# Performance work log

Hardware: AMD Instinct MI355X
Metric: run time of the kernel (lower is better)

## Reference

```python
import jax, jax.numpy as jnp
import numpy as np

L = 4       # num_fourier_layers
W = 256     # width
NF = 256    # num_freq (no_low_freq)
B = 2       # batch size
N = 16384   # num_nodes per graph
E = 524288  # total edges (avg degree 16)
D_IN = 3    # darcy input features


def lin(x, w, b):
    # torch nn.Linear convention: w is (out, in)
    return x @ w.T + b


def layernorm(x, s, b):
    m = x.mean(-1, keepdims=True)
    v = x.var(-1, keepdims=True)
    return (x - m) / jnp.sqrt(v + 1e-5) * s + b


def setup_inputs() -> dict:
    key = jax.random.key(0)
    ks = jax.random.split(key, 16)
    s = lambda i, shape, sc=0.05: sc * jax.random.normal(ks[i], shape, jnp.float32)
    inp = {
        "x": jax.random.normal(ks[0], (B * N, D_IN), jnp.float32),
        "U": jax.random.normal(ks[1], (B, N, NF), jnp.float32) / np.float32(np.sqrt(N)),
        "edge_index": jax.random.randint(ks[2], (2, E), 0, B * N),
        "edge_weight": jax.random.uniform(ks[3], (E,), jnp.float32),
        "lif_embed": jax.random.normal(ks[4], (B * N, 16), jnp.float32),
        "p_w": s(5, (W, D_IN)), "p_b": jnp.zeros((W,), jnp.float32),
        # scale = 1/(in*out) * rand, per GraphFourierLayer
        "four_w": (1.0 / (W * W)) * jax.random.uniform(ks[6], (L, W, W, NF), jnp.float32),
        "w_w": s(7, (L, W, W)), "w_b": jnp.zeros((L, W), jnp.float32),
        "ln_s": jnp.ones((L, W), jnp.float32), "ln_b": jnp.zeros((L, W), jnp.float32),
        "lin_w": s(8, (L, W, W)), "lin_b": jnp.zeros((L, W), jnp.float32),
        "ew_w": s(9, (L, 16, 1)), "ew_b": jnp.zeros((L, 16), jnp.float32),
        "g1_w": s(10, (L, 3, 48)), "g1_b": jnp.zeros((L, 3), jnp.float32),
        "g2_w": s(11, (L, 1, 3)), "g2_b": jnp.zeros((L, 1), jnp.float32),
        "proj_w": s(12, (W, 2 * W)), "proj_b": jnp.zeros((W,), jnp.float32),
        "q1_w": s(13, (128, W)), "q1_b": jnp.zeros((128,), jnp.float32),
        "q2_w": s(14, (1, 128)), "q2_b": jnp.zeros((1,), jnp.float32),
    }
    return inp


def reference(x, U, edge_index, edge_weight, lif_embed,
              p_w, p_b, four_w, w_w, w_b, ln_s, ln_b,
              lin_w, lin_b, ew_w, ew_b, g1_w, g1_b, g2_w, g2_b,
              proj_w, proj_b, q1_w, q1_b, q2_w, q2_b):
    src = edge_index[0]  # edge_index_j (source)
    dst = edge_index[1]  # edge_index_i (target, aggr='add')
    h = lin(x, p_w, p_b)  # [B*N, W]

    for l in range(L):
        # --- GraphFourierLayer: batched spectral transform ---
        h3 = h.reshape(B, N, W)
        x_ft = jnp.einsum('bnf,bnw->bfw', U, h3)          # U^T x  -> [B, NF, W]
        out_ft = jnp.einsum('bfi,iof->bfo', x_ft, four_w[l])
        x1 = jnp.einsum('bnf,bfw->bnw', U, out_ft).reshape(B * N, W)
        xf = jax.nn.gelu(x1 + lin(h, w_w[l], w_b[l]), approximate=False)
        xf = layernorm(xf, ln_s[l], ln_b[l])

        # --- FrigateConv: gather -> edge MLP gate -> scatter-add -> L2 normalize ---
        xs = lin(h, lin_w[l], lin_b[l])
        ew = lin(edge_weight[:, None], ew_w[l], ew_b[l])  # [E, 16]
        gin = jnp.concatenate([ew, lif_embed[dst], lif_embed[src]], axis=1)  # [E, 48]
        g = jax.nn.sigmoid(lin(jax.nn.relu(lin(gin, g1_w[l], g1_b[l])), g2_w[l], g2_b[l]))
        msg = xs[src] * g                                  # [E, W]
        agg = jax.ops.segment_sum(msg, dst, num_segments=B * N)
        nrm = jnp.maximum(jnp.linalg.norm(agg, axis=-1, keepdims=True), 1e-12)
        xs = agg / nrm

        h = lin(jnp.concatenate([xf, xs], axis=1), proj_w, proj_b)

    out = lin(jax.nn.relu(lin(h, q1_w, q1_b)), q2_w, q2_b)  # q: MLP(W,1,128)
    return out
```

## Files before the change

kernel.cpp:

```cpp
#include <hip/hip_runtime.h>
#include <hip/hip_bf16.h>

#define B_ 2
#define N_ 16384
#define BN 32768
#define W_ 256
#define NF_ 256
#define E_ 524288
#define L_ 4
#define KS_ 32

typedef __attribute__((ext_vector_type(8))) short bf16x8;
typedef __attribute__((ext_vector_type(4))) float f32x4;

__device__ __forceinline__ unsigned short f2b(float x) {
    __hip_bfloat16 h = __float2bfloat16(x);
    return *reinterpret_cast<unsigned short*>(&h);
}
__device__ __forceinline__ float b2f(unsigned short u) {
    union { unsigned int i; float f; } c; c.i = ((unsigned int)u) << 16; return c.f;
}
__device__ __forceinline__ float geluf(float x) {
    return 0.5f * x * (1.0f + erff(x * 0.70710678118654752440f));
}

template<bool DUAL, int OUTM, bool BIAS, bool QHEAD = false, bool TROUT = false>
__global__ __launch_bounds__(256) void k_mfma_nt(
    const unsigned short* __restrict__ A1, int lda1, long A1o, long A1i,
    const unsigned short* __restrict__ B1, int ldb1, long B1o, long B1i, int K1,
    const unsigned short* __restrict__ A2, int lda2, long A2o,
    const unsigned short* __restrict__ B2, int ldb2, long B2o, int K2,
    void* __restrict__ Cv, int ldc, long Co, long Ci,
    unsigned short* __restrict__ CT,
    const float* __restrict__ bias,
    const float* __restrict__ qw, const float* __restrict__ q2b,
    float* __restrict__ qout, int zdiv)
{
    __shared__ unsigned short lds[16384];
    const int t = threadIdx.x;
    const int wid = t >> 6, lane = t & 63;
    const int wr = wid >> 1, wc = wid & 1;
    const int m0 = blockIdx.y * 128, n0 = blockIdx.x * 128;
    const int z = blockIdx.z;
    const int zo = z / zdiv, zi = z - zo * zdiv;
    A1 += zo * A1o + zi * A1i;
    B1 += zo * B1o + zi * B1i;
    if (DUAL) { A2 += zo * A2o; B2 += zo * B2o; }

    const int srow  = t >> 3;
    const int sgran = (t & 7) ^ (srow & 7);
    const int rlo   = lane & 15;
    const int hi    = lane >> 4;

    f32x4 acc[4][4] = {};

    const int nph = DUAL ? 2 : 1;
    for (int ph = 0; ph < nph; ++ph) {
        const unsigned short* A  = (DUAL && ph) ? A2 : A1;
        const unsigned short* Bp = (DUAL && ph) ? B2 : B1;
        const int lda = (DUAL && ph) ? lda2 : lda1;
        const int ldb = (DUAL && ph) ? ldb2 : ldb1;
        const int K   = (DUAL && ph) ? K2 : K1;
        for (int k0 = 0; k0 < K; k0 += 64) {
            __syncthreads();
            #pragma unroll
            for (int j = 0; j < 4; ++j) {
                const unsigned short* ga = A + (long)(m0 + j*32 + srow) * lda + k0 + sgran*8;
                __builtin_amdgcn_global_load_lds(
                    (const __attribute__((address_space(1))) void*)ga,
                    (__attribute__((address_space(3))) void*)&lds[(j*4 + wid) * 512],
                    16, 0, 0);
            }
            #pragma unroll
            for (int j = 0; j < 4; ++j) {
                const unsigned short* gb = Bp + (long)(n0 + j*32 + srow) * ldb + k0 + sgran*8;
                __builtin_amdgcn_global_load_lds(
                    (const __attribute__((address_space(1))) void*)gb,
                    (__attribute__((address_space(3))) void*)&lds[8192 + (j*4 + wid) * 512],
                    16, 0, 0);
            }
            __syncthreads();
            #pragma unroll
            for (int kk = 0; kk < 2; ++kk) {
                const int g8 = (((kk*4 + hi) ^ (lane & 7)) << 3);
                bf16x8 a[4], b[4];
                #pragma unroll
                for (int fm = 0; fm < 4; ++fm)
                    a[fm] = *(const bf16x8*)&lds[(wr*64 + fm*16 + rlo)*64 + g8];
                #pragma unroll
                for (int fn = 0; fn < 4; ++fn)
                    b[fn] = *(const bf16x8*)&lds[8192 + (wc*64 + fn*16 + rlo)*64 + g8];
                #pragma unroll
                for (int fm = 0; fm < 4; ++fm)
                    #pragma unroll
                    for (int fn = 0; fn < 4; ++fn)
                        acc[fm][fn] = __builtin_amdgcn_mfma_f32_16x16x32_bf16(
                            a[fm], b[fn], acc[fm][fn], 0, 0, 0);
            }
        }
    }

    const int mb = m0 + wr*64, nb = n0 + wc*64;
    if (QHEAD) {
        __syncthreads();
        float* rs = (float*)lds;
        if (t < 128) rs[t] = 0.f;
        __syncthreads();
        #pragma unroll
        for (int fm = 0; fm < 4; ++fm)
            #pragma unroll
            for (int r = 0; r < 4; ++r) {
                const int m_l = wr*64 + fm*16 + hi*4 + r;
                float part = 0.f;
                #pragma unroll
                for (int fn = 0; fn < 4; ++fn) {
                    const int n = nb + fn*16 + rlo;
                    part += fmaxf(acc[fm][fn][r] + bias[n], 0.f) * qw[n];
                }
                #pragma unroll
                for (int o = 8; o; o >>= 1) part += __shfl_xor(part, o);
                if (rlo == 0) atomicAdd(&rs[m_l], part);
            }
        __syncthreads();
        if (t < 128) qout[m0 + t] = rs[t] + q2b[0];
    } else if (OUTM == 1) {
        unsigned short* C = (unsigned short*)Cv + zo * Co + zi * Ci;
        #pragma unroll
        for (int fn = 0; fn < 4; ++fn) {
            const int n = nb + fn*16 + rlo;
            const float bv = BIAS ? bias[n] : 0.f;
            #pragma unroll
            for (int fm = 0; fm < 4; ++fm)
                #pragma unroll
                for (int r = 0; r < 4; ++r) {
                    const int m = mb + fm*16 + hi*4 + r;
                    C[(long)m*ldc + n] = f2b(acc[fm][fn][r] + bv);
                }
        }
        if (TROUT) {
            __syncthreads();
            unsigned short* wlds = &lds[wid * 4096];
            #pragma unroll
            for (int fm = 0; fm < 4; ++fm)
                #pragma unroll
                for (int r = 0; r < 4; ++r) {
                    const int m_l = fm*16 + hi*4 + r;
                    const int sw = (m_l & 7) << 3;
                    #pragma unroll
                    for (int fn = 0; fn < 4; ++fn) {
                        const int n_l = fn*16 + rlo;
                        const float bv = BIAS ? bias[nb + n_l] : 0.f;
                        wlds[m_l*64 + (n_l ^ sw)] = f2b(acc[fm][fn][r] + bv);
                    }
                }
            const int bb = mb >> 14, loc = mb & 16383;
            const int mq = lane & 15, nq = lane >> 4;
            #pragma unroll
            for (int p = 0; p < 16; ++p) {
                const int n_l = p*4 + nq;
                unsigned short v[4];
                #pragma unroll
                for (int j = 0; j < 4; ++j) {
                    const int m_l = mq*4 + j;
                    v[j] = wlds[m_l*64 + (n_l ^ ((m_l & 7) << 3))];
                }
                *(ushort4*)&CT[((long)bb*ldc + nb + n_l)*N_ + loc + mq*4] = *(ushort4*)v;
            }
        }
    } else {
        float* C = (float*)Cv + zo * Co + zi * Ci;
        #pragma unroll
        for (int fn = 0; fn < 4; ++fn) {
            const int n = nb + fn*16 + rlo;
            const float bv = BIAS ? bias[n] : 0.f;
            #pragma unroll
            for (int fm = 0; fm < 4; ++fm)
                #pragma unroll
                for (int r = 0; r < 4; ++r) {
                    const int m = mb + fm*16 + hi*4 + r;
                    C[(long)m*ldc + n] = acc[fm][fn][r] + bv;
                }
        }
    }
}

__global__ __launch_bounds__(256) void k_cvt_all(
    const float* __restrict__ w, const float* __restrict__ lin,
    const float* __restrict__ proj, const float* __restrict__ q1,
    unsigned short* __restrict__ wd, unsigned short* __restrict__ lind,
    unsigned short* __restrict__ projd, unsigned short* __restrict__ q1d)
{
    const int b = blockIdx.x;
    const float* s; unsigned short* d; long base;
    if (b < 256)      { s = w;    d = wd;    base = (long)b * 1024; }
    else if (b < 512) { s = lin;  d = lind;  base = (long)(b-256) * 1024; }
    else if (b < 640) { s = proj; d = projd; base = (long)(b-512) * 1024; }
    else              { s = q1;   d = q1d;   base = (long)(b-640) * 1024; }
    long i = base + (long)threadIdx.x * 4;
    float4 v = *(const float4*)&s[i];
    ushort4 u = {f2b(v.x), f2b(v.y), f2b(v.z), f2b(v.w)};
    *(ushort4*)&d[i] = u;
}

__global__ __launch_bounds__(256) void k_cvtT(
    const float* __restrict__ src, unsigned short* __restrict__ dT, unsigned short* __restrict__ dL)
{
    const int b = blockIdx.z;
    src += (long)b * N_ * NF_; dT += (long)b * N_ * NF_; dL += (long)b * N_ * NF_;
    const int r0 = blockIdx.y * 64, c0 = blockIdx.x * 64;
    __shared__ unsigned short tile[64][72];
    const int t = threadIdx.x, lr = t >> 4, lc4 = (t & 15) * 4;
    #pragma unroll
    for (int p = 0; p < 4; ++p) {
        int r = p*16 + lr;
        float4 v = *(const float4*)&src[(long)(r0+r)*NF_ + c0 + lc4];
        ushort4 u = {f2b(v.x), f2b(v.y), f2b(v.z), f2b(v.w)};
        *(ushort4*)&dL[(long)(r0+r)*NF_ + c0 + lc4] = u;
        tile[r][lc4+0]=u.x; tile[r][lc4+1]=u.y; tile[r][lc4+2]=u.z; tile[r][lc4+3]=u.w;
    }
    __syncthreads();
    #pragma unroll
    for (int p = 0; p < 4; ++p) {
        int c = p*16 + lr;
        ushort4 u = {tile[lc4+0][c], tile[lc4+1][c], tile[lc4+2][c], tile[lc4+3][c]};
        *(ushort4*)&dT[(long)(c0+c)*N_ + r0 + lc4] = u;
    }
}

__global__ __launch_bounds__(256) void k_T_b2b(
    const unsigned short* __restrict__ src, unsigned short* __restrict__ dst)
{
    const int b = blockIdx.z;
    src += (long)b * N_ * W_; dst += (long)b * N_ * W_;
    const int r0 = blockIdx.y * 64, c0 = blockIdx.x * 64;
    __shared__ unsigned short tile[64][72];
    const int t = threadIdx.x, lr = t >> 4, lc4 = (t & 15) * 4;
    #pragma unroll
    for (int p = 0; p < 4; ++p) {
        int r = p*16 + lr;
        ushort4 v = *(const ushort4*)&src[(long)(r0+r)*W_ + c0 + lc4];
        tile[r][lc4+0]=v.x; tile[r][lc4+1]=v.y; tile[r][lc4+2]=v.z; tile[r][lc4+3]=v.w;
    }
    __syncthreads();
    #pragma unroll
    for (int p = 0; p < 4; ++p) {
        int c = p*16 + lr;
        ushort4 u = {tile[lc4+0][c], tile[lc4+1][c], tile[lc4+2][c], tile[lc4+3][c]};
        *(ushort4*)&dst[(long)(c0+c)*N_ + r0 + lc4] = u;
    }
}

__global__ __launch_bounds__(256) void k_in_proj(
    const float* __restrict__ x, const float* __restrict__ pw,
    const float* __restrict__ pb, unsigned short* __restrict__ h)
{
    int idx = blockIdx.x * 256 + threadIdx.x;
    int node = idx >> 8, w = idx & 255;
    float x0 = x[node*3+0], x1 = x[node*3+1], x2 = x[node*3+2];
    h[idx] = f2b(fmaf(x0, pw[w*3+0], fmaf(x1, pw[w*3+1], fmaf(x2, pw[w*3+2], pb[w]))));
}

__global__ __launch_bounds__(256) void k_reduce_ks(
    const float* __restrict__ part, float* __restrict__ outp)
{
    int idx = blockIdx.x * 256 + threadIdx.x;
    int b = idx >> 16, rem = idx & 65535;
    const float* p = part + (long)b * KS_ * 65536 + rem;
    float s = 0.f;
    #pragma unroll
    for (int k = 0; k < KS_; ++k) s += p[(long)k * 65536];
    outp[idx] = s;
}

__global__ __launch_bounds__(256) void k_fourier_mul(
    const float* __restrict__ fw, const float* __restrict__ xftT,
    unsigned short* __restrict__ oftT)
{
    const int o = blockIdx.x, f = threadIdx.x;
    const float* fwp = fw + (long)o * NF_ + f;
    float a0 = 0.f, a1 = 0.f;
    #pragma unroll 8
    for (int i = 0; i < W_; ++i) {
        float w = fwp[(long)i * W_ * NF_];
        a0 = fmaf(xftT[i*NF_ + f], w, a0);
        a1 = fmaf(xftT[65536 + i*NF_ + f], w, a1);
    }
    oftT[o*NF_ + f] = f2b(a0);
    oftT[65536 + o*NF_ + f] = f2b(a1);
}

__global__ __launch_bounds__(256) void k_gelu_ln(
    const unsigned short* __restrict__ xf, unsigned short* __restrict__ out,
    const float* __restrict__ wb, const float* __restrict__ lns, const float* __restrict__ lnb)
{
    const int node = blockIdx.x * 4 + (threadIdx.x >> 6);
    const int lane = threadIdx.x & 63;
    ushort4 v4 = *(const ushort4*)(xf + (long)node*W_ + lane*4);
    float4 bb = *(const float4*)(wb + lane*4);
    float e0 = geluf(b2f(v4.x)+bb.x), e1 = geluf(b2f(v4.y)+bb.y);
    float e2 = geluf(b2f(v4.z)+bb.z), e3 = geluf(b2f(v4.w)+bb.w);
    float s  = e0+e1+e2+e3;
    float s2 = e0*e0+e1*e1+e2*e2+e3*e3;
    #pragma unroll
    for (int o = 32; o; o >>= 1) { s += __shfl_xor(s, o); s2 += __shfl_xor(s2, o); }
    float mean = s * (1.0f/W_);
    float var  = s2 * (1.0f/W_) - mean*mean;
    float inv = rsqrtf(var + 1e-5f);
    float4 sc = *(const float4*)(lns + lane*4);
    float4 bi = *(const float4*)(lnb + lane*4);
    ushort4 o4;
    o4.x = f2b((e0-mean)*inv*sc.x + bi.x);
    o4.y = f2b((e1-mean)*inv*sc.y + bi.y);
    o4.z = f2b((e2-mean)*inv*sc.z + bi.z);
    o4.w = f2b((e3-mean)*inv*sc.w + bi.w);
    *(ushort4*)(out + (long)node*W_ + lane*4) = o4;
}

__global__ __launch_bounds__(256) void k_hist(const int* __restrict__ ei, int* __restrict__ count) {
    int e = blockIdx.x * 256 + threadIdx.x;
    atomicAdd(&count[ei[E_ + e]], 1);
}
__global__ __launch_bounds__(256) void k_scan(const int* __restrict__ count, int* __restrict__ offsets) {
    __shared__ int sums[256];
    const int t = threadIdx.x;
    const int base = t * 128;
    int s = 0;
    for (int i = 0; i < 128; ++i) s += count[base + i];
    sums[t] = s;
    __syncthreads();
    for (int off = 1; off < 256; off <<= 1) {
        int v = (t >= off) ? sums[t - off] : 0;
        __syncthreads();
        sums[t] += v;
        __syncthreads();
    }
    int run = (t == 0) ? 0 : sums[t - 1];
    for (int i = 0; i < 128; ++i) { offsets[base + i] = run; run += count[base + i]; }
    if (t == 255) offsets[BN] = run;
}
__global__ __launch_bounds__(256) void k_place(
    const int* __restrict__ ei, const float* __restrict__ ewt,
    const int* __restrict__ offsets, int* __restrict__ cursor,
    int* __restrict__ srcp, float* __restrict__ ewt_p)
{
    int e = blockIdx.x * 256 + threadIdx.x;
    int dst = ei[E_ + e];
    int pos = offsets[dst] + atomicAdd(&cursor[dst], 1);
    srcp[pos] = ei[e];
    ewt_p[pos] = ewt[e];
}

__global__ __launch_bounds__(256) void k_gate_agg(
    const int* __restrict__ offsets, const int* __restrict__ srcp,
    const float* __restrict__ ewt_p, const float* __restrict__ lif,
    const float* __restrict__ eww, const float* __restrict__ ewb,
    const float* __restrict__ g1w, const float* __restrict__ g1b,
    const float* __restrict__ g2w, const float* __restrict__ g2b,
    const unsigned short* __restrict__ xs, unsigned short* __restrict__ out)
{
    const int node = blockIdx.x * 4 + (threadIdx.x >> 6);
    const int lane = threadIdx.x & 63;
    const int beg = offsets[node], end = offsets[node + 1];
    float lifd[16];
    #pragma unroll
    for (int j = 0; j < 16; ++j) lifd[j] = lif[node*16 + j];
    float a0=0.f, a1=0.f, a2=0.f, a3=0.f;
    for (int c0 = beg; c0 < end; c0 += 64) {
        const int p = c0 + lane;
        float gate = 0.f; int src = 0;
        if (p < end) {
            src = srcp[p];
            const float wv = ewt_p[p];
            float t0 = g1b[0], t1 = g1b[1], t2 = g1b[2];
            #pragma unroll
            for (int j = 0; j < 16; ++j) {
                const float e0 = fmaf(wv, eww[j], ewb[j]);
                const float l1 = lifd[j];
                const float l2 = lif[src*16 + j];
                t0 = fmaf(g1w[j], e0, t0);
                t0 = fmaf(g1w[16 + j], l1, t0);
                t0 = fmaf(g1w[32 + j], l2, t0);
                t1 = fmaf(g1w[48 + j], e0, t1);
                t1 = fmaf(g1w[64 + j], l1, t1);
                t1 = fmaf(g1w[80 + j], l2, t1);
                t2 = fmaf(g1w[96 + j], e0, t2);
                t2 = fmaf(g1w[112 + j], l1, t2);
                t2 = fmaf(g1w[128 + j], l2, t2);
            }
            float z = g2b[0];
            z = fmaf(g2w[0], fmaxf(t0, 0.f), z);
            z = fmaf(g2w[1], fmaxf(t1, 0.f), z);
            z = fmaf(g2w[2], fmaxf(t2, 0.f), z);
            gate = 1.f / (1.f + __expf(-z));
        }
        const int m = min(64, end - c0);
        for (int j = 0; j < m; ++j) {
            const float gv = __shfl(gate, j);
            const int   s  = __shfl(src, j);
            ushort4 v = *(const ushort4*)&xs[(long)s * W_ + lane * 4];
            a0 = fmaf(b2f(v.x), gv, a0);
            a1 = fmaf(b2f(v.y), gv, a1);
            a2 = fmaf(b2f(v.z), gv, a2);
            a3 = fmaf(b2f(v.w), gv, a3);
        }
    }
    float s = a0*a0 + a1*a1 + a2*a2 + a3*a3;
    #pragma unroll
    for (int o = 32; o; o >>= 1) s += __shfl_xor(s, o);
    float inv = 1.f / fmaxf(sqrtf(s), 1e-12f);
    ushort4 r = {f2b(a0*inv), f2b(a1*inv), f2b(a2*inv), f2b(a3*inv)};
    *(ushort4*)(out + (long)node * W_ + lane * 4) = r;
}

extern "C" void kernel_launch(void* const* d_in, const int* in_sizes, int n_in,
                              void* d_out, int out_size, void* d_ws, size_t ws_size,
                              hipStream_t stream)
{
    const float* x      = (const float*)d_in[0];
    const float* U      = (const float*)d_in[1];
    const int*   ei     = (const int*)  d_in[2];
    const float* ewt    = (const float*)d_in[3];
    const float* lif    = (const float*)d_in[4];
    const float* p_w    = (const float*)d_in[5];
    const float* p_b    = (const float*)d_in[6];
    const float* four_w = (const float*)d_in[7];
    const float* w_w    = (const float*)d_in[8];
    const float* w_b    = (const float*)d_in[9];
    const float* ln_s   = (const float*)d_in[10];
    const float* ln_b   = (const float*)d_in[11];
    const float* lin_w  = (const float*)d_in[12];
    const float* lin_b  = (const float*)d_in[13];
    const float* ew_w   = (const float*)d_in[14];
    const float* ew_b   = (const float*)d_in[15];
    const float* g1_w   = (const float*)d_in[16];
    const float* g1_b   = (const float*)d_in[17];
    const float* g2_w   = (const float*)d_in[18];
    const float* g2_b   = (const float*)d_in[19];
    const float* proj_w = (const float*)d_in[20];
    const float* proj_b = (const float*)d_in[21];
    const float* q1_w   = (const float*)d_in[22];
    const float* q1_b   = (const float*)d_in[23];
    const float* q2_w   = (const float*)d_in[24];
    const float* q2_b   = (const float*)d_in[25];

    char* wsb = (char*)d_ws;
    size_t off = 0;
    auto alloc = [&](size_t bytes) -> void* {
        void* p = wsb + off; off += (bytes + 255) & ~(size_t)255; return p;
    };
    float* xft_part  = (float*)alloc((size_t)B_ * KS_ * 65536 * 4);
    float* xftT      = (float*)alloc((size_t)B_ * 65536 * 4);
    unsigned short* h_bf   = (unsigned short*)alloc((size_t)BN * W_ * 2);
    unsigned short* hT_bf  = (unsigned short*)alloc((size_t)BN * W_ * 2);
    unsigned short* U_bf   = (unsigned short*)alloc((size_t)BN * NF_ * 2);
    unsigned short* UT_bf  = (unsigned short*)alloc((size_t)BN * NF_ * 2);
    unsigned short* xfg    = (unsigned short*)alloc((size_t)BN * W_ * 2);
    unsigned short* xf_bf  = (unsigned short*)alloc((size_t)BN * W_ * 2);
    unsigned short* xs_bf  = (unsigned short*)alloc((size_t)BN * W_ * 2);
    unsigned short* xsn_bf = (unsigned short*)alloc((size_t)BN * W_ * 2);
    unsigned short* oftT_bf= (unsigned short*)alloc((size_t)B_ * 65536 * 2);
    unsigned short* wwb    = (unsigned short*)alloc((size_t)L_ * W_ * W_ * 2);
    unsigned short* linwb  = (unsigned short*)alloc((size_t)L_ * W_ * W_ * 2);
    unsigned short* projwb = (unsigned short*)alloc((size_t)W_ * 2 * W_ * 2);
    unsigned short* q1wb   = (unsigned short*)alloc((size_t)128 * W_ * 2);
    int*   srcp    = (int*)alloc((size_t)E_ * 4);
    float* ewt_p   = (float*)alloc((size_t)E_ * 4);
    int*   count   = (int*)alloc((size_t)BN * 4);
    int*   cursor  = (int*)alloc((size_t)BN * 4);
    int*   offsets = (int*)alloc((size_t)(BN + 1) * 4);

    hipMemsetAsync(count, 0, (size_t)2 * BN * 4, stream);
    k_hist<<<E_/256, 256, 0, stream>>>(ei, count);
    k_scan<<<1, 256, 0, stream>>>(count, offsets);
    k_place<<<E_/256, 256, 0, stream>>>(ei, ewt, offsets, cursor, srcp, ewt_p);

    k_cvt_all<<<672, 256, 0, stream>>>(w_w, lin_w, proj_w, q1_w, wwb, linwb, projwb, q1wb);
    k_cvtT<<<dim3(NF_/64, N_/64, B_), 256, 0, stream>>>(U, UT_bf, U_bf);

    k_in_proj<<<BN, 256, 0, stream>>>(x, p_w, p_b, h_bf);
    k_T_b2b<<<dim3(W_/64, N_/64, B_), 256, 0, stream>>>(h_bf, hT_bf);

    for (int l = 0; l < L_; ++l) {
        k_mfma_nt<false,0,false><<<dim3(2, 2, B_*KS_), 256, 0, stream>>>(
            hT_bf, N_, (long)W_*N_, N_/KS_,
            UT_bf, N_, (long)NF_*N_, N_/KS_, N_/KS_,
            nullptr, 0, 0, nullptr, 0, 0, 0,
            xft_part, NF_, (long)KS_*65536, 65536,
            nullptr, nullptr, nullptr, nullptr, nullptr, KS_);
        k_reduce_ks<<<(B_*65536)/256, 256, 0, stream>>>(xft_part, xftT);
        k_fourier_mul<<<W_, 256, 0, stream>>>(four_w + (long)l*W_*W_*NF_, xftT, oftT_bf);
        k_mfma_nt<true,1,false><<<dim3(2, N_/128, B_), 256, 0, stream>>>(
            U_bf, NF_, (long)N_*NF_, 0,
            oftT_bf, NF_, (long)65536, 0, NF_,
            h_bf, W_, (long)N_*W_,
            wwb + (long)l*W_*W_, W_, 0, W_,
            xfg, W_, (long)N_*W_, 0,
            nullptr, nullptr, nullptr, nullptr, nullptr, 1);
        k_gelu_ln<<<BN/4, 256, 0, stream>>>(xfg, xf_bf, w_b + l*W_, ln_s + l*W_, ln_b + l*W_);
        k_mfma_nt<false,1,true><<<dim3(2, BN/128, 1), 256, 0, stream>>>(
            h_bf, W_, 0, 0,
            linwb + (long)l*W_*W_, W_, 0, 0, W_,
            nullptr, 0, 0, nullptr, 0, 0, 0,
            xs_bf, W_, 0, 0,
            nullptr, lin_b + l*W_, nullptr, nullptr, nullptr, 1);
        k_gate_agg<<<BN/4, 256, 0, stream>>>(offsets, srcp, ewt_p, lif,
            ew_w + l*16, ew_b + l*16, g1_w + l*144, g1_b + l*3,
            g2_w + l*3, g2_b + l, xs_bf, xsn_bf);
        if (l < 3) {
            k_mfma_nt<true,1,true,false,true><<<dim3(2, BN/128, 1), 256, 0, stream>>>(
                xf_bf, W_, 0, 0,
                projwb, 2*W_, 0, 0, W_,
                xsn_bf, W_, 0,
                projwb + W_, 2*W_, 0, W_,
                h_bf, W_, 0, 0,
                hT_bf, proj_b, nullptr, nullptr, nullptr, 1);
        } else {
            k_mfma_nt<true,1,true><<<dim3(2, BN/128, 1), 256, 0, stream>>>(
                xf_bf, W_, 0, 0,
                projwb, 2*W_, 0, 0, W_,
                xsn_bf, W_, 0,
                projwb + W_, 2*W_, 0, W_,
                h_bf, W_, 0, 0,
                nullptr, proj_b, nullptr, nullptr, nullptr, 1);
        }
    }
    k_mfma_nt<false,0,true,true><<<dim3(1, BN/128, 1), 256, 0, stream>>>(
        h_bf, W_, 0, 0,
        q1wb, W_, 0, 0, W_,
        nullptr, 0, 0, nullptr, 0, 0, 0,
        nullptr, 128, 0, 0,
        nullptr, q1_b, q2_w, q2_b, (float*)d_out, 1);
}
```

Before: 816.0 us.

## Fuse spectral-inverse, w_w and lin_w GEMMs into one kernel; raise split-K

Adds a dedicated MFMA kernel that computes U·out_ft + h·w_wᵀ and h·lin_wᵀ + bias in one pass. It loads each h tile into LDS once and feeds two accumulator sets, replacing two separate GEMM launches. This removes a second read of h and one kernel launch per layer. The cost is more registers for the dual accumulators and more LDS traffic. Separately, the split-K factor for the U^T·h reduction doubles, which increases parallelism but also doubles the partial-sum buffer and the work in the reduction kernel.

Result: no change. 827.3 us (+1.4%).

```diff
diff --git a/kernel.cpp b/kernel.cpp
--- a/kernel.cpp
+++ b/kernel.cpp
@@ -8,7 +8,7 @@
 #define NF_ 256
 #define E_ 524288
 #define L_ 4
-#define KS_ 32
+#define KS_ 64
 
 typedef __attribute__((ext_vector_type(8))) short bf16x8;
 typedef __attribute__((ext_vector_type(4))) float f32x4;
@@ -184,6 +184,124 @@
     }
 }
 
+__global__ __launch_bounds__(256) void k_mfma_layer(
+    const unsigned short* __restrict__ Ubf, const unsigned short* __restrict__ oftT,
+    const unsigned short* __restrict__ h,
+    const unsigned short* __restrict__ ww, const unsigned short* __restrict__ linw,
+    const float* __restrict__ lin_b,
+    unsigned short* __restrict__ xf, unsigned short* __restrict__ xs)
+{
+    __shared__ unsigned short lds[24576];
+    const int t = threadIdx.x;
+    const int wid = t >> 6, lane = t & 63;
+    const int wr = wid >> 1, wc = wid & 1;
+    const int m0 = blockIdx.y * 128, n0 = blockIdx.x * 128;
+    const int b = blockIdx.z;
+    Ubf  += (long)b * N_ * NF_;
+    oftT += (long)b * 65536;
+    h    += (long)b * N_ * W_;
+
+    const int srow  = t >> 3;
+    const int sgran = (t & 7) ^ (srow & 7);
+    const int rlo   = lane & 15;
+    const int hi    = lane >> 4;
+
+    f32x4 acc1[4][4] = {};
+    f32x4 acc2[4][4] = {};
+
+    for (int k0 = 0; k0 < NF_; k0 += 64) {
+        __syncthreads();
+        #pragma unroll
+        for (int j = 0; j < 4; ++j) {
+            const unsigned short* ga = Ubf + (long)(m0 + j*32 + srow) * NF_ + k0 + sgran*8;
+            __builtin_amdgcn_global_load_lds(
+                (const __attribute__((address_space(1))) void*)ga,
+                (__attribute__((address_space(3))) void*)&lds[(j*4 + wid) * 512], 16, 0, 0);
+            const unsigned short* gb = oftT + (long)(n0 + j*32 + srow) * NF_ + k0 + sgran*8;
+            __builtin_amdgcn_global_load_lds(
+                (const __attribute__((address_space(1))) void*)gb,
+                (__attribute__((address_space(3))) void*)&lds[8192 + (j*4 + wid) * 512], 16, 0, 0);
+        }
+        __syncthreads();
+        #pragma unroll
+        for (int kk = 0; kk < 2; ++kk) {
+            const int g8 = (((kk*4 + hi) ^ (lane & 7)) << 3);
+            bf16x8 a[4], b1[4];
+            #pragma unroll
+            for (int fm = 0; fm < 4; ++fm)
+                a[fm] = *(const bf16x8*)&lds[(wr*64 + fm*16 + rlo)*64 + g8];
+            #pragma unroll
+            for (int fn = 0; fn < 4; ++fn)
+                b1[fn] = *(const bf16x8*)&lds[8192 + (wc*64 + fn*16 + rlo)*64 + g8];
+            #pragma unroll
+            for (int fm = 0; fm < 4; ++fm)
+                #pragma unroll
+                for (int fn = 0; fn < 4; ++fn)
+                    acc1[fm][fn] = __builtin_amdgcn_mfma_f32_16x16x32_bf16(
+                        a[fm], b1[fn], acc1[fm][fn], 0, 0, 0);
+        }
+    }
+
+    for (int k0 = 0; k0 < W_; k0 += 64) {
+        __syncthreads();
+        #pragma unroll
+        for (int j = 0; j < 4; ++j) {
+            const unsigned short* ga = h + (long)(m0 + j*32 + srow) * W_ + k0 + sgran*8;
+            __builtin_amdgcn_global_load_lds(
+                (const __attribute__((address_space(1))) void*)ga,
+                (__attribute__((address_space(3))) void*)&lds[(j*4 + wid) * 512], 16, 0, 0);
+            const unsigned short* gb1 = ww + (long)(n0 + j*32 + srow) * W_ + k0 + sgran*8;
+            __builtin_amdgcn_global_load_lds(
+                (const __attribute__((address_space(1))) void*)gb1,
+                (__attribute__((address_space(3))) void*)&lds[8192 + (j*4 + wid) * 512], 16, 0, 0);
+            const unsigned short* gb2 = linw + (long)(n0 + j*32 + srow) * W_ + k0 + sgran*8;
+            __builtin_amdgcn_global_load_lds(
+                (const __attribute__((address_space(1))) void*)gb2,
+                (__attribute__((address_space(3))) void*)&lds[16384 + (j*4 + wid) * 512], 16, 0, 0);
+        }
+        __syncthreads();
+        #pragma unroll
+        for (int kk = 0; kk < 2; ++kk) {
+            const int g8 = (((kk*4 + hi) ^ (lane & 7)) << 3);
+            bf16x8 a[4], b1[4], b2[4];
+            #pragma unroll
+            for (int fm = 0; fm < 4; ++fm)
+                a[fm] = *(const bf16x8*)&lds[(wr*64 + fm*16 + rlo)*64 + g8];
+            #pragma unroll
+            for (int fn = 0; fn < 4; ++fn) {
+                b1[fn] = *(const bf16x8*)&lds[8192  + (wc*64 + fn*16 + rlo)*64 + g8];
+                b2[fn] = *(const bf16x8*)&lds[16384 + (wc*64 + fn*16 + rlo)*64 + g8];
+            }
+            #pragma unroll
+            for (int fm = 0; fm < 4; ++fm)
+                #pragma unroll
+                for (int fn = 0; fn < 4; ++fn) {
+                    acc1[fm][fn] = __builtin_amdgcn_mfma_f32_16x16x32_bf16(
+                        a[fm], b1[fn], acc1[fm][fn], 0, 0, 0);
+                    acc2[fm][fn] = __builtin_amdgcn_mfma_f32_16x16x32_bf16(
+                        a[fm], b2[fn], acc2[fm][fn], 0, 0, 0);
+                }
+        }
+    }
+
+    const int mb = m0 + wr*64, nb = n0 + wc*64;
+    unsigned short* C1 = xf + (long)b * N_ * W_;
+    unsigned short* C2 = xs + (long)b * N_ * W_;
+    #pragma unroll
+    for (int fn = 0; fn < 4; ++fn) {
+        const int n = nb + fn*16 + rlo;
+        const float lb = lin_b[n];
+        #pragma unroll
+        for (int fm = 0; fm < 4; ++fm)
+            #pragma unroll
+            for (int r = 0; r < 4; ++r) {
+                const int m = mb + fm*16 + hi*4 + r;
+                C1[(long)m*W_ + n] = f2b(acc1[fm][fn][r]);
+                C2[(long)m*W_ + n] = f2b(acc2[fm][fn][r] + lb);
+            }
+    }
+}
+
 __global__ __launch_bounds__(256) void k_cvt_all(
     const float* __restrict__ w, const float* __restrict__ lin,
     const float* __restrict__ proj, const float* __restrict__ q1,
@@ -267,7 +385,7 @@
     int b = idx >> 16, rem = idx & 65535;
     const float* p = part + (long)b * KS_ * 65536 + rem;
     float s = 0.f;
-    #pragma unroll
+    #pragma unroll 16
     for (int k = 0; k < KS_; ++k) s += p[(long)k * 65536];
     outp[idx] = s;
 }
@@ -489,20 +607,11 @@
             nullptr, nullptr, nullptr, nullptr, nullptr, KS_);
         k_reduce_ks<<<(B_*65536)/256, 256, 0, stream>>>(xft_part, xftT);
         k_fourier_mul<<<W_, 256, 0, stream>>>(four_w + (long)l*W_*W_*NF_, xftT, oftT_bf);
-        k_mfma_nt<true,1,false><<<dim3(2, N_/128, B_), 256, 0, stream>>>(
-            U_bf, NF_, (long)N_*NF_, 0,
-            oftT_bf, NF_, (long)65536, 0, NF_,
-            h_bf, W_, (long)N_*W_,
-            wwb + (long)l*W_*W_, W_, 0, W_,
-            xfg, W_, (long)N_*W_, 0,
-            nullptr, nullptr, nullptr, nullptr, nullptr, 1);
+        k_mfma_layer<<<dim3(2, N_/128, B_), 256, 0, stream>>>(
+            U_bf, oftT_bf, h_bf,
+            wwb + (long)l*W_*W_, linwb + (long)l*W_*W_, lin_b + l*W_,
+            xfg, xs_bf);
         k_gelu_ln<<<BN/4, 256, 0, stream>>>(xfg, xf_bf, w_b + l*W_, ln_s + l*W_, ln_b + l*W_);
-        k_mfma_nt<false,1,true><<<dim3(2, BN/128, 1), 256, 0, stream>>>(
-            h_bf, W_, 0, 0,
-            linwb + (long)l*W_*W_, W_, 0, 0, W_,
-            nullptr, 0, 0, nullptr, 0, 0, 0,
-            xs_bf, W_, 0, 0,
-            nullptr, lin_b + l*W_, nullptr, nullptr, nullptr, 1);
         k_gate_agg<<<BN/4, 256, 0, stream>>>(offsets, srcp, ewt_p, lif,
             ew_w + l*16, ew_b + l*16, g1_w + l*144, g1_b + l*3,
             g2_w + l*3, g2_b + l, xs_bf, xsn_bf);
```
